# Optimization experiments

Hardware: AMD Instinct MI355X
Metric: run time of the kernel (lower is better)

## Reference

```python
import jax, jax.numpy as jnp
import numpy as np

MAX_NODES = 1024
FEAT = 64
HID = 32
B, S = 32, 4096


def setup_inputs() -> dict:
    key = jax.random.key(0)
    ks = jax.random.split(key, 9)
    flow_features = jax.random.normal(ks[0], (B, S, FEAT), dtype=jnp.float32)
    src_ips = jax.random.randint(ks[1], (B, S), 0, MAX_NODES, dtype=jnp.int32)
    dst_ips = jax.random.randint(ks[2], (B, S), 0, MAX_NODES, dtype=jnp.int32)
    flow_volumes = jax.random.uniform(ks[3], (B, S), dtype=jnp.float32)
    # learned parameters
    node_emb = jax.random.normal(ks[4], (MAX_NODES, FEAT), dtype=jnp.float32)
    W1 = jax.random.normal(ks[5], (2 * FEAT, HID), dtype=jnp.float32) * (1.0 / np.sqrt(2 * FEAT))
    b1 = jnp.zeros((HID,), dtype=jnp.float32)
    W2 = jax.random.normal(ks[6], (HID, 1), dtype=jnp.float32) * (1.0 / np.sqrt(HID))
    b2 = jnp.zeros((1,), dtype=jnp.float32)
    return {"flow_features": flow_features, "src_ips": src_ips, "dst_ips": dst_ips,
            "flow_volumes": flow_volumes, "node_emb": node_emb,
            "W1": W1, "b1": b1, "W2": W2, "b2": b2}


def reference(flow_features, src_ips, dst_ips, flow_volumes, node_emb, W1, b1, W2, b2):
    b_, s_, f_ = flow_features.shape
    n_ = node_emb.shape[0]
    bidx = jnp.arange(b_)[:, None]  # (B,1) broadcast over seq

    # ---- scatter-add flow features into destination nodes ----
    node_features = jnp.zeros((b_, n_, f_), dtype=flow_features.dtype)
    node_features = node_features.at[bidx, dst_ips].add(flow_features)
    # F.normalize(p=2, dim=-1): x / max(||x||, eps)
    norm = jnp.linalg.norm(node_features, axis=-1, keepdims=True)
    node_features = node_features / jnp.maximum(norm, 1e-12)

    # ---- gather embeddings, edge MLP, scatter weights into adjacency ----
    src_e = node_emb[src_ips]  # (B,S,F)
    dst_e = node_emb[dst_ips]  # (B,S,F)
    h = jax.nn.relu(jnp.concatenate([src_e, dst_e], axis=-1) @ W1 + b1)  # (B,S,32)
    edge_w = jax.nn.sigmoid((h @ W2 + b2)[..., 0])  # (B,S)
    vol_w = jax.nn.sigmoid(flow_volumes / 1000.0)
    w = edge_w * vol_w  # (B,S)

    adjacency = jnp.zeros((b_, n_, n_), dtype=flow_features.dtype)
    # semantics up to scatter ordering of colliding edges)
    adjacency = adjacency.at[bidx, src_ips, dst_ips].set(w)
    adjacency = adjacency.at[bidx, dst_ips, src_ips].set(w)
    return node_features, adjacency
```

## Files before the change

kernel.cpp:

```cpp
#include <hip/hip_runtime.h>
#include <cstdint>
#include <cstddef>

#define BB 32
#define SS 4096
#define FEAT_ 64
#define HID_ 32
#define NN 1024
#define RPB 8

#define EDGE_BLOCKS ((BB * SS) / 256)
#define NF_BLOCKS   ((BB * NN) / 32)

typedef int v4i __attribute__((ext_vector_type(4)));

__global__ void ab_kernel(const float* __restrict__ emb,
                          const float* __restrict__ W1,
                          const float* __restrict__ b1,
                          float* __restrict__ ab) {
    int idx = blockIdx.x * 256 + threadIdx.x;
    int n = idx >> 6;
    int c = idx & 63;
    int half = c >> 5, j = c & 31;
    const float* e = emb + (n << 6);
    const float* w = W1 + (half << 11) + j;
    float acc = half ? 0.0f : b1[j];
    #pragma unroll
    for (int k = 0; k < 64; ++k)
        acc = fmaf(e[k], w[k << 5], acc);
    ab[idx] = acc;
}

__global__ void nf_edge_kernel(const float* __restrict__ flow,
                               const int* __restrict__ src,
                               const int* __restrict__ dst,
                               const float* __restrict__ vol,
                               const float* __restrict__ ab,
                               const float* __restrict__ W2,
                               const float* __restrict__ b2,
                               float* __restrict__ nf,
                               float* __restrict__ wout) {
    if (blockIdx.x < EDGE_BLOCKS) {
        int i = blockIdx.x * 256 + threadIdx.x;
        int si = src[i], di = dst[i];
        const float4* As = (const float4*)(ab + (si << 6));
        const float4* Bd = (const float4*)(ab + (di << 6) + HID_);
        float dotv = b2[0];
        #pragma unroll
        for (int q = 0; q < 8; ++q) {
            float4 a  = As[q];
            float4 bv = Bd[q];
            float4 wv = *(const float4*)(W2 + (q << 2));
            dotv += fmaxf(a.x + bv.x, 0.0f) * wv.x;
            dotv += fmaxf(a.y + bv.y, 0.0f) * wv.y;
            dotv += fmaxf(a.z + bv.z, 0.0f) * wv.z;
            dotv += fmaxf(a.w + bv.w, 0.0f) * wv.w;
        }
        float edge_w = 1.0f / (1.0f + expf(-dotv));
        float vol_w  = 1.0f / (1.0f + expf(-vol[i] / 1000.0f));
        wout[i] = edge_w * vol_w;
        return;
    }

    int nb = blockIdx.x - EDGE_BLOCKS;
    int row0 = nb << 5;
    int b = row0 >> 10;
    __shared__ int sdst[SS];

    const int4* g = (const int4*)(dst + (size_t)b * SS);
    int4* sd4 = (int4*)sdst;
    for (int t = threadIdx.x; t < SS / 4; t += 256) sd4[t] = g[t];
    __syncthreads();

    int wave = threadIdx.x >> 6;
    int lane = threadIdx.x & 63;
    int r0 = row0 + (wave << 3);
    int node0 = r0 & (NN - 1);
    const float* fb = flow + ((size_t)b * SS << 6);

    float acc[8] = {0.f, 0.f, 0.f, 0.f, 0.f, 0.f, 0.f, 0.f};
    for (int s0 = 0; s0 < SS; s0 += 64) {
        int d = sdst[s0 + lane];
        #pragma unroll
        for (int j = 0; j < 8; ++j) {
            unsigned long long m = __ballot(d == node0 + j);
            while (m) {
                int bit = __ffsll((long long)m) - 1;
                m &= m - 1;
                acc[j] += fb[((s0 + bit) << 6) + lane];
            }
        }
    }

    #pragma unroll
    for (int j = 0; j < 8; ++j) {
        float ss = acc[j] * acc[j];
        #pragma unroll
        for (int off = 32; off > 0; off >>= 1) ss += __shfl_xor(ss, off, 64);
        float v = acc[j] / fmaxf(sqrtf(ss), 1e-12f);
        __builtin_nontemporal_store(v, &nf[((size_t)(r0 + j) << 6) + lane]);
    }
}

__global__ void adj_dense_kernel(const int* __restrict__ src,
                                 const int* __restrict__ dst,
                                 const float* __restrict__ wbuf,
                                 float* __restrict__ adj) {
    int b  = blockIdx.x >> 7;
    int r0 = (blockIdx.x & 127) << 3;
    int tid = threadIdx.x;

    __shared__ int D[RPB * NN];

    const int* sb = src + (size_t)b * SS;
    const int* db = dst + (size_t)b * SS;
    int svr[16], dvr[16];
    #pragma unroll
    for (int i = 0; i < 16; ++i) {
        svr[i] = sb[tid + (i << 8)];
        dvr[i] = db[tid + (i << 8)];
    }

    int4* D4 = (int4*)D;
    int4 z; z.x = z.y = z.z = z.w = 0;
    #pragma unroll
    for (int i = 0; i < RPB * NN / 4 / 256; ++i) D4[tid + i * 256] = z;
    __syncthreads();

    #pragma unroll
    for (int i = 0; i < 16; ++i) {
        int s = tid + (i << 8);
        unsigned lr1 = (unsigned)(svr[i] - r0);
        if (lr1 < RPB) atomicMax(&D[(lr1 << 10) + dvr[i]], s + 1);
        unsigned lr2 = (unsigned)(dvr[i] - r0);
        if (lr2 < RPB) atomicMax(&D[(lr2 << 10) + svr[i]], SS + s + 1);
    }
    __syncthreads();

    const float* wb = wbuf + (size_t)b * SS;
    #pragma unroll
    for (int i = 0; i < 16; ++i) {
        int s = tid + (i << 8);
        unsigned lr1 = (unsigned)(svr[i] - r0);
        unsigned lr2 = (unsigned)(dvr[i] - r0);
        if ((lr1 < RPB) | (lr2 < RPB)) {
            int wbits = __float_as_int(wb[s]);
            if (lr1 < RPB && D[(lr1 << 10) + dvr[i]] == s + 1)
                D[(lr1 << 10) + dvr[i]] = wbits;
            if (lr2 < RPB && D[(lr2 << 10) + svr[i]] == SS + s + 1)
                D[(lr2 << 10) + svr[i]] = wbits;
        }
    }
    __syncthreads();

    const v4i* Df = (const v4i*)D;
    v4i* out = (v4i*)(adj + ((size_t)b * NN + r0) * NN);
    #pragma unroll
    for (int i = 0; i < RPB * NN / 4 / 256; ++i)
        __builtin_nontemporal_store(Df[tid + i * 256], &out[tid + i * 256]);
}

extern "C" void kernel_launch(void* const* d_in, const int* in_sizes, int n_in,
                              void* d_out, int out_size, void* d_ws, size_t ws_size,
                              hipStream_t stream) {
    const float* flow = (const float*)d_in[0];
    const int*   src  = (const int*)d_in[1];
    const int*   dst  = (const int*)d_in[2];
    const float* vol  = (const float*)d_in[3];
    const float* emb  = (const float*)d_in[4];
    const float* W1   = (const float*)d_in[5];
    const float* b1   = (const float*)d_in[6];
    const float* W2   = (const float*)d_in[7];
    const float* b2   = (const float*)d_in[8];

    float* nf   = (float*)d_out;
    float* adj  = nf + (size_t)BB * NN * FEAT_;
    float* wbuf = (float*)d_ws;

    float* ab;
    if (ws_size >= (size_t)(BB * SS + NN * 64) * sizeof(float))
        ab = wbuf + (size_t)BB * SS;
    else
        ab = adj + (size_t)BB * NN * NN - (size_t)NN * 64;

    ab_kernel<<<(NN * 64) / 256, 256, 0, stream>>>(emb, W1, b1, ab);
    nf_edge_kernel<<<EDGE_BLOCKS + NF_BLOCKS, 256, 0, stream>>>(
        flow, src, dst, vol, ab, W2, b2, nf, wbuf);
    adj_dense_kernel<<<BB * (NN / RPB), 256, 0, stream>>>(src, dst, wbuf, adj);
}
```

Measured before the change: 225.5 us.

## Build CSR edge lists per node and fuse scatter-add with adjacency construction

A setup kernel computes the embedding projections and builds per-batch CSR (counting sort) edge lists keyed by dst and by src. The dst list is insertion-sorted so sums keep sequence order. A single fused kernel then computes node features by walking only the incident edges, and fills adjacency tiles by visiting only the edges in each row range, computing edge weights on demand. This replaces the O(S) ballot scan per row group and the full-edge scan per adjacency block, and drops the separate edge-weight pass and a kernel launch. In exchange it adds sorting overhead, serial insertion sort in some threads, and a larger workspace requirement, with the old path kept as a fallback.

```diff
diff --git a/kernel.cpp b/kernel.cpp
--- a/kernel.cpp
+++ b/kernel.cpp
@@ -14,20 +14,238 @@
 
 typedef int v4i __attribute__((ext_vector_type(4)));
 
+__device__ __forceinline__ float edge_weight(const float* __restrict__ ab,
+                                             const float* __restrict__ W2,
+                                             float b2v, int src_n, int dst_n,
+                                             float volv) {
+    const float4* As = (const float4*)(ab + (src_n << 6));
+    const float4* Bd = (const float4*)(ab + (dst_n << 6) + HID_);
+    float dotv = b2v;
+    #pragma unroll
+    for (int q = 0; q < 8; ++q) {
+        float4 a  = As[q];
+        float4 bv = Bd[q];
+        float4 wv = *(const float4*)(W2 + (q << 2));
+        dotv += fmaxf(a.x + bv.x, 0.0f) * wv.x;
+        dotv += fmaxf(a.y + bv.y, 0.0f) * wv.y;
+        dotv += fmaxf(a.z + bv.z, 0.0f) * wv.z;
+        dotv += fmaxf(a.w + bv.w, 0.0f) * wv.w;
+    }
+    float edge_w = 1.0f / (1.0f + expf(-dotv));
+    float vol_w  = 1.0f / (1.0f + expf(-volv / 1000.0f));
+    return edge_w * vol_w;
+}
+
+__global__ void setup_kernel(const float* __restrict__ emb,
+                             const float* __restrict__ W1,
+                             const float* __restrict__ b1,
+                             const int* __restrict__ src,
+                             const int* __restrict__ dst,
+                             float* __restrict__ ab,
+                             int* __restrict__ offD, int* __restrict__ idxD,
+                             int* __restrict__ offS, int* __restrict__ idxS) {
+    int t = threadIdx.x;
+    if (blockIdx.x < 256) {
+        int idx = blockIdx.x * 256 + t;
+        int n = idx >> 6, c = idx & 63;
+        int half = c >> 5, j = c & 31;
+        const float* e = emb + (n << 6);
+        const float* w = W1 + (half << 11) + j;
+        float acc = half ? 0.0f : b1[j];
+        #pragma unroll
+        for (int k = 0; k < 64; ++k) acc = fmaf(e[k], w[k << 5], acc);
+        ab[idx] = acc;
+        return;
+    }
+
+    int blk = blockIdx.x - 256;
+    int dir = blk >> 5;
+    int b   = blk & 31;
+    const int* keyg = (dir ? src : dst) + (size_t)b * SS;
+    const int* othg = (dir ? dst : src) + (size_t)b * SS;
+    int* offg = (dir ? offS : offD) + b * (NN + 1);
+    int* idxg = (dir ? idxS : idxD) + b * SS;
+
+    int kv[16], ov[16];
+    #pragma unroll
+    for (int i = 0; i < 16; ++i) {
+        kv[i] = keyg[t + (i << 8)];
+        ov[i] = othg[t + (i << 8)];
+    }
+
+    __shared__ int cnt[NN];
+    __shared__ int wtot[4];
+    #pragma unroll
+    for (int i = 0; i < 4; ++i) cnt[(t << 2) + i] = 0;
+    __syncthreads();
+    #pragma unroll
+    for (int i = 0; i < 16; ++i) atomicAdd(&cnt[kv[i]], 1);
+    __syncthreads();
+
+    int c0 = cnt[t * 4], c1 = cnt[t * 4 + 1], c2 = cnt[t * 4 + 2], c3 = cnt[t * 4 + 3];
+    int p1 = c0 + c1, p2 = p1 + c2, p3 = p2 + c3;
+    int x = p3;
+    int lane = t & 63, wv = t >> 6;
+    #pragma unroll
+    for (int d = 1; d < 64; d <<= 1) {
+        int y = __shfl_up(x, d, 64);
+        if (lane >= d) x += y;
+    }
+    if (lane == 63) wtot[wv] = x;
+    __syncthreads();
+    int wbase = 0;
+    #pragma unroll
+    for (int w2 = 0; w2 < 4; ++w2) if (w2 < wv) wbase += wtot[w2];
+    int e0 = wbase + x - p3;
+    int e1 = e0 + c0, e2 = e0 + p1, e3 = e0 + p2;
+    offg[t * 4 + 0] = e0; offg[t * 4 + 1] = e1;
+    offg[t * 4 + 2] = e2; offg[t * 4 + 3] = e3;
+    if (t == 255) offg[NN] = SS;
+    __syncthreads();
+    cnt[t * 4] = e0; cnt[t * 4 + 1] = e1; cnt[t * 4 + 2] = e2; cnt[t * 4 + 3] = e3;
+    __syncthreads();
+
+    #pragma unroll
+    for (int i = 0; i < 16; ++i) {
+        int s = t + (i << 8);
+        int pos = atomicAdd(&cnt[kv[i]], 1);
+        idxg[pos] = (int)((unsigned)s | ((unsigned)ov[i] << 12) | ((unsigned)kv[i] << 22));
+    }
+
+    if (dir == 0) {
+        __syncthreads();
+        int beg[4] = {e0, e1, e2, e3};
+        int len[4] = {c0, c1, c2, c3};
+        #pragma unroll
+        for (int q = 0; q < 4; ++q) {
+            int lo = beg[q], hi = beg[q] + len[q];
+            for (int p = lo + 1; p < hi; ++p) {
+                int v = idxg[p];
+                int sq = v & 4095;
+                int r = p - 1;
+                while (r >= lo && (idxg[r] & 4095) > sq) { idxg[r + 1] = idxg[r]; --r; }
+                idxg[r + 1] = v;
+            }
+        }
+    }
+}
+
+__global__ void fused_kernel(const float* __restrict__ flow,
+                             const float* __restrict__ vol,
+                             const float* __restrict__ ab,
+                             const float* __restrict__ W2,
+                             const float* __restrict__ b2,
+                             const int* __restrict__ offD, const int* __restrict__ idxD,
+                             const int* __restrict__ offS, const int* __restrict__ idxS,
+                             float* __restrict__ nf,
+                             float* __restrict__ adj) {
+    int g = blockIdx.x / 5;
+    int r = blockIdx.x - g * 5;
+    int t = threadIdx.x;
+    __shared__ int D[RPB * NN];
+
+    if (r == 4) {
+        int nb = g;
+        int b = nb >> 5;
+        int row0 = (nb & 31) << 5;
+        int wave = t >> 6, lane = t & 63;
+        int r0 = row0 + (wave << 3);
+        const float* fb = flow + ((size_t)b * SS << 6);
+        const int* offb = offD + b * (NN + 1);
+        const int* idxb = idxD + b * SS;
+        #pragma unroll
+        for (int j = 0; j < 8; ++j) {
+            int row = r0 + j;
+            int eb = offb[row], ee = offb[row + 1];
+            float a = 0.f;
+            int e = eb;
+            for (; e + 4 <= ee; e += 4) {
+                int s0 = idxb[e]     & 4095, s1 = idxb[e + 1] & 4095;
+                int s2 = idxb[e + 2] & 4095, s3 = idxb[e + 3] & 4095;
+                float v0 = fb[(s0 << 6) + lane], v1 = fb[(s1 << 6) + lane];
+                float v2 = fb[(s2 << 6) + lane], v3 = fb[(s3 << 6) + lane];
+                a = (((a + v0) + v1) + v2) + v3;
+            }
+            for (; e < ee; ++e) {
+                int s = idxb[e] & 4095;
+                a += fb[(s << 6) + lane];
+            }
+            float ssum = a * a;
+            #pragma unroll
+            for (int off = 32; off > 0; off >>= 1) ssum += __shfl_xor(ssum, off, 64);
+            float v = a / fmaxf(sqrtf(ssum), 1e-12f);
+            __builtin_nontemporal_store(
+                v, &nf[((size_t)(b * NN + row) << 6) + lane]);
+        }
+        return;
+    }
+
+    int aidx = g * 4 + r;
+    int b  = aidx >> 7;
+    int r0 = (aidx & 127) << 3;
+
+    const int* offSb = offS + b * (NN + 1);
+    const int* offDb = offD + b * (NN + 1);
+    const int* idxSb = idxS + b * SS;
+    const int* idxDb = idxD + b * SS;
+    int begS = offSb[r0], cntS = offSb[r0 + RPB] - begS;
+    int begD = offDb[r0], cntD = offDb[r0 + RPB] - begD;
+
+    int4* D4 = (int4*)D;
+    int4 z; z.x = z.y = z.z = z.w = 0;
+    #pragma unroll
+    for (int i = 0; i < RPB * NN / 4 / 256; ++i) D4[t + i * 256] = z;
+    __syncthreads();
+
+    for (int i = t; i < cntS; i += 256) {
+        unsigned v = (unsigned)idxSb[begS + i];
+        int s = (int)(v & 4095u); int col = (int)((v >> 12) & 1023u); int row = (int)(v >> 22);
+        atomicMax(&D[((row - r0) << 10) + col], s + 1);
+    }
+    for (int i = t; i < cntD; i += 256) {
+        unsigned v = (unsigned)idxDb[begD + i];
+        int s = (int)(v & 4095u); int col = (int)((v >> 12) & 1023u); int row = (int)(v >> 22);
+        atomicMax(&D[((row - r0) << 10) + col], SS + s + 1);
+    }
+    __syncthreads();
+
+    const float* volb = vol + (size_t)b * SS;
+    float b2v = b2[0];
+    for (int i = t; i < cntS; i += 256) {
+        unsigned v = (unsigned)idxSb[begS + i];
+        int s = (int)(v & 4095u); int col = (int)((v >> 12) & 1023u); int row = (int)(v >> 22);
+        int cell = ((row - r0) << 10) + col;
+        if (D[cell] == s + 1)
+            D[cell] = __float_as_int(edge_weight(ab, W2, b2v, row, col, volb[s]));
+    }
+    for (int i = t; i < cntD; i += 256) {
+        unsigned v = (unsigned)idxDb[begD + i];
+        int s = (int)(v & 4095u); int col = (int)((v >> 12) & 1023u); int row = (int)(v >> 22);
+        int cell = ((row - r0) << 10) + col;
+        if (D[cell] == SS + s + 1)
+            D[cell] = __float_as_int(edge_weight(ab, W2, b2v, col, row, volb[s]));
+    }
+    __syncthreads();
+
+    const v4i* Df = (const v4i*)D;
+    v4i* out = (v4i*)(adj + ((size_t)b * NN + r0) * NN);
+    #pragma unroll
+    for (int i = 0; i < RPB * NN / 4 / 256; ++i)
+        __builtin_nontemporal_store(Df[t + i * 256], &out[t + i * 256]);
+}
+
 __global__ void ab_kernel(const float* __restrict__ emb,
                           const float* __restrict__ W1,
                           const float* __restrict__ b1,
                           float* __restrict__ ab) {
     int idx = blockIdx.x * 256 + threadIdx.x;
-    int n = idx >> 6;
-    int c = idx & 63;
+    int n = idx >> 6, c = idx & 63;
     int half = c >> 5, j = c & 31;
     const float* e = emb + (n << 6);
     const float* w = W1 + (half << 11) + j;
     float acc = half ? 0.0f : b1[j];
     #pragma unroll
-    for (int k = 0; k < 64; ++k)
-        acc = fmaf(e[k], w[k << 5], acc);
+    for (int k = 0; k < 64; ++k) acc = fmaf(e[k], w[k << 5], acc);
     ab[idx] = acc;
 }
 
@@ -43,42 +261,23 @@
     if (blockIdx.x < EDGE_BLOCKS) {
         int i = blockIdx.x * 256 + threadIdx.x;
         int si = src[i], di = dst[i];
-        const float4* As = (const float4*)(ab + (si << 6));
-        const float4* Bd = (const float4*)(ab + (di << 6) + HID_);
-        float dotv = b2[0];
-        #pragma unroll
-        for (int q = 0; q < 8; ++q) {
-            float4 a  = As[q];
-            float4 bv = Bd[q];
-            float4 wv = *(const float4*)(W2 + (q << 2));
-            dotv += fmaxf(a.x + bv.x, 0.0f) * wv.x;
-            dotv += fmaxf(a.y + bv.y, 0.0f) * wv.y;
-            dotv += fmaxf(a.z + bv.z, 0.0f) * wv.z;
-            dotv += fmaxf(a.w + bv.w, 0.0f) * wv.w;
-        }
-        float edge_w = 1.0f / (1.0f + expf(-dotv));
-        float vol_w  = 1.0f / (1.0f + expf(-vol[i] / 1000.0f));
-        wout[i] = edge_w * vol_w;
+        float w = edge_weight(ab, W2, b2[0], si, di, vol[i]);
+        wout[i] = w;
         return;
     }
-
     int nb = blockIdx.x - EDGE_BLOCKS;
     int row0 = nb << 5;
     int b = row0 >> 10;
     __shared__ int sdst[SS];
-
     const int4* g = (const int4*)(dst + (size_t)b * SS);
     int4* sd4 = (int4*)sdst;
     for (int t = threadIdx.x; t < SS / 4; t += 256) sd4[t] = g[t];
     __syncthreads();
-
-    int wave = threadIdx.x >> 6;
-    int lane = threadIdx.x & 63;
+    int wave = threadIdx.x >> 6, lane = threadIdx.x & 63;
     int r0 = row0 + (wave << 3);
     int node0 = r0 & (NN - 1);
     const float* fb = flow + ((size_t)b * SS << 6);
-
-    float acc[8] = {0.f, 0.f, 0.f, 0.f, 0.f, 0.f, 0.f, 0.f};
+    float acc[8] = {0.f,0.f,0.f,0.f,0.f,0.f,0.f,0.f};
     for (int s0 = 0; s0 < SS; s0 += 64) {
         int d = sdst[s0 + lane];
         #pragma unroll
@@ -91,7 +290,6 @@
             }
         }
     }
-
     #pragma unroll
     for (int j = 0; j < 8; ++j) {
         float ss = acc[j] * acc[j];
@@ -109,24 +307,17 @@
     int b  = blockIdx.x >> 7;
     int r0 = (blockIdx.x & 127) << 3;
     int tid = threadIdx.x;
-
     __shared__ int D[RPB * NN];
-
     const int* sb = src + (size_t)b * SS;
     const int* db = dst + (size_t)b * SS;
     int svr[16], dvr[16];
     #pragma unroll
-    for (int i = 0; i < 16; ++i) {
-        svr[i] = sb[tid + (i << 8)];
-        dvr[i] = db[tid + (i << 8)];
-    }
-
+    for (int i = 0; i < 16; ++i) { svr[i] = sb[tid + (i << 8)]; dvr[i] = db[tid + (i << 8)]; }
     int4* D4 = (int4*)D;
     int4 z; z.x = z.y = z.z = z.w = 0;
     #pragma unroll
     for (int i = 0; i < RPB * NN / 4 / 256; ++i) D4[tid + i * 256] = z;
     __syncthreads();
-
     #pragma unroll
     for (int i = 0; i < 16; ++i) {
         int s = tid + (i << 8);
@@ -136,7 +327,6 @@
         if (lr2 < RPB) atomicMax(&D[(lr2 << 10) + svr[i]], SS + s + 1);
     }
     __syncthreads();
-
     const float* wb = wbuf + (size_t)b * SS;
     #pragma unroll
     for (int i = 0; i < 16; ++i) {
@@ -145,14 +335,11 @@
         unsigned lr2 = (unsigned)(dvr[i] - r0);
         if ((lr1 < RPB) | (lr2 < RPB)) {
             int wbits = __float_as_int(wb[s]);
-            if (lr1 < RPB && D[(lr1 << 10) + dvr[i]] == s + 1)
-                D[(lr1 << 10) + dvr[i]] = wbits;
-            if (lr2 < RPB && D[(lr2 << 10) + svr[i]] == SS + s + 1)
-                D[(lr2 << 10) + svr[i]] = wbits;
+            if (lr1 < RPB && D[(lr1 << 10) + dvr[i]] == s + 1) D[(lr1 << 10) + dvr[i]] = wbits;
+            if (lr2 < RPB && D[(lr2 << 10) + svr[i]] == SS + s + 1) D[(lr2 << 10) + svr[i]] = wbits;
         }
     }
     __syncthreads();
-
     const v4i* Df = (const v4i*)D;
     v4i* out = (v4i*)(adj + ((size_t)b * NN + r0) * NN);
     #pragma unroll
@@ -173,16 +360,30 @@
     const float* W2   = (const float*)d_in[7];
     const float* b2   = (const float*)d_in[8];
 
-    float* nf   = (float*)d_out;
-    float* adj  = nf + (size_t)BB * NN * FEAT_;
+    float* nf  = (float*)d_out;
+    float* adj = nf + (size_t)BB * NN * FEAT_;
+
+    size_t need = ((size_t)NN * 64 + 2 * (size_t)BB * (NN + 1) + 2 * (size_t)BB * SS)
+                  * sizeof(float);
+    if (ws_size >= need) {
+        float* ab  = (float*)d_ws;
+        int* offD = (int*)(ab + NN * 64);
+        int* idxD = offD + BB * (NN + 1);
+        int* offS = idxD + BB * SS;
+        int* idxS = offS + BB * (NN + 1);
+        setup_kernel<<<320, 256, 0, stream>>>(emb, W1, b1, src, dst,
+                                              ab, offD, idxD, offS, idxS);
+        fused_kernel<<<5120, 256, 0, stream>>>(flow, vol, ab, W2, b2,
+                                               offD, idxD, offS, idxS, nf, adj);
+        return;
+    }
+
     float* wbuf = (float*)d_ws;
-
     float* ab;
     if (ws_size >= (size_t)(BB * SS + NN * 64) * sizeof(float))
         ab = wbuf + (size_t)BB * SS;
     else
         ab = adj + (size_t)BB * NN * NN - (size_t)NN * 64;
-
     ab_kernel<<<(NN * 64) / 256, 256, 0, stream>>>(emb, W1, b1, ab);
     nf_edge_kernel<<<EDGE_BLOCKS + NF_BLOCKS, 256, 0, stream>>>(
         flow, src, dst, vol, ab, W2, b2, nf, wbuf);
```

Result: slower. 252.5 us (+12.0%).

## Fuse node-feature and adjacency kernels, compute edge weights inside adjacency blocks

Applied to the files above, without the earlier changes.

Merges the node-feature scatter and dense adjacency construction into a single launch, interleaving one node-feature block per four adjacency blocks. Edge weights are no longer precomputed into a workspace buffer; each adjacency block evaluates the edge MLP on demand for edges touching its rows. This removes one launch, the weight buffer round trip, and serialization between the two phases. In exchange, edges are evaluated about twice (once per endpoint row block), and the node-feature blocks now share the larger shared-memory footprint, which could lower occupancy.

```diff
diff --git a/kernel.cpp b/kernel.cpp
--- a/kernel.cpp
+++ b/kernel.cpp
@@ -14,21 +14,149 @@
 
 typedef int v4i __attribute__((ext_vector_type(4)));
 
+__device__ __forceinline__ float edge_weight(const float* __restrict__ ab,
+                                             const float* __restrict__ W2,
+                                             float b2v, int src_n, int dst_n,
+                                             float volv) {
+    const float4* As = (const float4*)(ab + (src_n << 6));
+    const float4* Bd = (const float4*)(ab + (dst_n << 6) + HID_);
+    float dotv = b2v;
+    #pragma unroll
+    for (int q = 0; q < 8; ++q) {
+        float4 a  = As[q];
+        float4 bv = Bd[q];
+        float4 wv = *(const float4*)(W2 + (q << 2));
+        dotv += fmaxf(a.x + bv.x, 0.0f) * wv.x;
+        dotv += fmaxf(a.y + bv.y, 0.0f) * wv.y;
+        dotv += fmaxf(a.z + bv.z, 0.0f) * wv.z;
+        dotv += fmaxf(a.w + bv.w, 0.0f) * wv.w;
+    }
+    float edge_w = 1.0f / (1.0f + expf(-dotv));
+    float vol_w  = 1.0f / (1.0f + expf(-volv / 1000.0f));
+    return edge_w * vol_w;
+}
+
 __global__ void ab_kernel(const float* __restrict__ emb,
                           const float* __restrict__ W1,
                           const float* __restrict__ b1,
                           float* __restrict__ ab) {
     int idx = blockIdx.x * 256 + threadIdx.x;
-    int n = idx >> 6;
-    int c = idx & 63;
+    int n = idx >> 6, c = idx & 63;
     int half = c >> 5, j = c & 31;
     const float* e = emb + (n << 6);
     const float* w = W1 + (half << 11) + j;
     float acc = half ? 0.0f : b1[j];
     #pragma unroll
-    for (int k = 0; k < 64; ++k)
-        acc = fmaf(e[k], w[k << 5], acc);
+    for (int k = 0; k < 64; ++k) acc = fmaf(e[k], w[k << 5], acc);
     ab[idx] = acc;
+}
+
+__global__ void fused2_kernel(const float* __restrict__ flow,
+                              const int* __restrict__ src,
+                              const int* __restrict__ dst,
+                              const float* __restrict__ vol,
+                              const float* __restrict__ ab,
+                              const float* __restrict__ W2,
+                              const float* __restrict__ b2,
+                              float* __restrict__ nf,
+                              float* __restrict__ adj) {
+    int g = blockIdx.x / 5;
+    int r = blockIdx.x - g * 5;
+    int t = threadIdx.x;
+    __shared__ int D[RPB * NN];
+
+    if (r == 4) {
+        int nb = g;
+        int row0 = nb << 5;
+        int b = row0 >> 10;
+        int* sdst = D;
+
+        const int4* gsrc = (const int4*)(dst + (size_t)b * SS);
+        int4* sd4 = (int4*)sdst;
+        for (int i = t; i < SS / 4; i += 256) sd4[i] = gsrc[i];
+        __syncthreads();
+
+        int wave = t >> 6, lane = t & 63;
+        int r0 = row0 + (wave << 3);
+        int node0 = r0 & (NN - 1);
+        const float* fb = flow + ((size_t)b * SS << 6);
+
+        float acc[8] = {0.f,0.f,0.f,0.f,0.f,0.f,0.f,0.f};
+        for (int s0 = 0; s0 < SS; s0 += 64) {
+            int d = sdst[s0 + lane];
+            #pragma unroll
+            for (int j = 0; j < 8; ++j) {
+                unsigned long long m = __ballot(d == node0 + j);
+                while (m) {
+                    int bit = __ffsll((long long)m) - 1;
+                    m &= m - 1;
+                    acc[j] += fb[((s0 + bit) << 6) + lane];
+                }
+            }
+        }
+        #pragma unroll
+        for (int j = 0; j < 8; ++j) {
+            float ss = acc[j] * acc[j];
+            #pragma unroll
+            for (int off = 32; off > 0; off >>= 1) ss += __shfl_xor(ss, off, 64);
+            float v = acc[j] / fmaxf(sqrtf(ss), 1e-12f);
+            __builtin_nontemporal_store(v, &nf[((size_t)(r0 + j) << 6) + lane]);
+        }
+        return;
+    }
+
+    int aidx = g * 4 + r;
+    int b  = aidx >> 7;
+    int r0 = (aidx & 127) << 3;
+
+    const int* sb = src + (size_t)b * SS;
+    const int* db = dst + (size_t)b * SS;
+    int svr[16], dvr[16];
+    #pragma unroll
+    for (int i = 0; i < 16; ++i) {
+        svr[i] = sb[t + (i << 8)];
+        dvr[i] = db[t + (i << 8)];
+    }
+
+    int4* D4 = (int4*)D;
+    int4 z; z.x = z.y = z.z = z.w = 0;
+    #pragma unroll
+    for (int i = 0; i < RPB * NN / 4 / 256; ++i) D4[t + i * 256] = z;
+    __syncthreads();
+
+    #pragma unroll
+    for (int i = 0; i < 16; ++i) {
+        int s = t + (i << 8);
+        unsigned lr1 = (unsigned)(svr[i] - r0);
+        if (lr1 < RPB) atomicMax(&D[(lr1 << 10) + dvr[i]], s + 1);
+        unsigned lr2 = (unsigned)(dvr[i] - r0);
+        if (lr2 < RPB) atomicMax(&D[(lr2 << 10) + svr[i]], SS + s + 1);
+    }
+    __syncthreads();
+
+    const float* volb = vol + (size_t)b * SS;
+    float b2v = b2[0];
+    #pragma unroll
+    for (int i = 0; i < 16; ++i) {
+        int s = t + (i << 8);
+        unsigned lr1 = (unsigned)(svr[i] - r0);
+        unsigned lr2 = (unsigned)(dvr[i] - r0);
+        if ((lr1 < RPB) | (lr2 < RPB)) {
+            float w = edge_weight(ab, W2, b2v, svr[i], dvr[i], volb[s]);
+            int wbits = __float_as_int(w);
+            if (lr1 < RPB && D[(lr1 << 10) + dvr[i]] == s + 1)
+                D[(lr1 << 10) + dvr[i]] = wbits;
+            if (lr2 < RPB && D[(lr2 << 10) + svr[i]] == SS + s + 1)
+                D[(lr2 << 10) + svr[i]] = wbits;
+        }
+    }
+    __syncthreads();
+
+    const v4i* Df = (const v4i*)D;
+    v4i* out = (v4i*)(adj + ((size_t)b * NN + r0) * NN);
+    #pragma unroll
+    for (int i = 0; i < RPB * NN / 4 / 256; ++i)
+        __builtin_nontemporal_store(Df[t + i * 256], &out[t + i * 256]);
 }
 
 __global__ void nf_edge_kernel(const float* __restrict__ flow,
@@ -42,43 +170,23 @@
                                float* __restrict__ wout) {
     if (blockIdx.x < EDGE_BLOCKS) {
         int i = blockIdx.x * 256 + threadIdx.x;
-        int si = src[i], di = dst[i];
-        const float4* As = (const float4*)(ab + (si << 6));
-        const float4* Bd = (const float4*)(ab + (di << 6) + HID_);
-        float dotv = b2[0];
-        #pragma unroll
-        for (int q = 0; q < 8; ++q) {
-            float4 a  = As[q];
-            float4 bv = Bd[q];
-            float4 wv = *(const float4*)(W2 + (q << 2));
-            dotv += fmaxf(a.x + bv.x, 0.0f) * wv.x;
-            dotv += fmaxf(a.y + bv.y, 0.0f) * wv.y;
-            dotv += fmaxf(a.z + bv.z, 0.0f) * wv.z;
-            dotv += fmaxf(a.w + bv.w, 0.0f) * wv.w;
-        }
-        float edge_w = 1.0f / (1.0f + expf(-dotv));
-        float vol_w  = 1.0f / (1.0f + expf(-vol[i] / 1000.0f));
-        wout[i] = edge_w * vol_w;
+        float w = edge_weight(ab, W2, b2[0], src[i], dst[i], vol[i]);
+        wout[i] = w;
         return;
     }
-
     int nb = blockIdx.x - EDGE_BLOCKS;
     int row0 = nb << 5;
     int b = row0 >> 10;
     __shared__ int sdst[SS];
-
     const int4* g = (const int4*)(dst + (size_t)b * SS);
     int4* sd4 = (int4*)sdst;
     for (int t = threadIdx.x; t < SS / 4; t += 256) sd4[t] = g[t];
     __syncthreads();
-
-    int wave = threadIdx.x >> 6;
-    int lane = threadIdx.x & 63;
+    int wave = threadIdx.x >> 6, lane = threadIdx.x & 63;
     int r0 = row0 + (wave << 3);
     int node0 = r0 & (NN - 1);
     const float* fb = flow + ((size_t)b * SS << 6);
-
-    float acc[8] = {0.f, 0.f, 0.f, 0.f, 0.f, 0.f, 0.f, 0.f};
+    float acc[8] = {0.f,0.f,0.f,0.f,0.f,0.f,0.f,0.f};
     for (int s0 = 0; s0 < SS; s0 += 64) {
         int d = sdst[s0 + lane];
         #pragma unroll
@@ -91,7 +199,6 @@
             }
         }
     }
-
     #pragma unroll
     for (int j = 0; j < 8; ++j) {
         float ss = acc[j] * acc[j];
@@ -109,24 +216,17 @@
     int b  = blockIdx.x >> 7;
     int r0 = (blockIdx.x & 127) << 3;
     int tid = threadIdx.x;
-
     __shared__ int D[RPB * NN];
-
     const int* sb = src + (size_t)b * SS;
     const int* db = dst + (size_t)b * SS;
     int svr[16], dvr[16];
     #pragma unroll
-    for (int i = 0; i < 16; ++i) {
-        svr[i] = sb[tid + (i << 8)];
-        dvr[i] = db[tid + (i << 8)];
-    }
-
+    for (int i = 0; i < 16; ++i) { svr[i] = sb[tid + (i << 8)]; dvr[i] = db[tid + (i << 8)]; }
     int4* D4 = (int4*)D;
     int4 z; z.x = z.y = z.z = z.w = 0;
     #pragma unroll
     for (int i = 0; i < RPB * NN / 4 / 256; ++i) D4[tid + i * 256] = z;
     __syncthreads();
-
     #pragma unroll
     for (int i = 0; i < 16; ++i) {
         int s = tid + (i << 8);
@@ -136,7 +236,6 @@
         if (lr2 < RPB) atomicMax(&D[(lr2 << 10) + svr[i]], SS + s + 1);
     }
     __syncthreads();
-
     const float* wb = wbuf + (size_t)b * SS;
     #pragma unroll
     for (int i = 0; i < 16; ++i) {
@@ -145,14 +244,11 @@
         unsigned lr2 = (unsigned)(dvr[i] - r0);
         if ((lr1 < RPB) | (lr2 < RPB)) {
             int wbits = __float_as_int(wb[s]);
-            if (lr1 < RPB && D[(lr1 << 10) + dvr[i]] == s + 1)
-                D[(lr1 << 10) + dvr[i]] = wbits;
-            if (lr2 < RPB && D[(lr2 << 10) + svr[i]] == SS + s + 1)
-                D[(lr2 << 10) + svr[i]] = wbits;
-        }
-    }
-    __syncthreads();
-
+            if (lr1 < RPB && D[(lr1 << 10) + dvr[i]] == s + 1) D[(lr1 << 10) + dvr[i]] = wbits;
+            if (lr2 < RPB && D[(lr2 << 10) + svr[i]] == SS + s + 1) D[(lr2 << 10) + svr[i]] = wbits;
+        }
+    }
+    __syncthreads();
     const v4i* Df = (const v4i*)D;
     v4i* out = (v4i*)(adj + ((size_t)b * NN + r0) * NN);
     #pragma unroll
@@ -173,16 +269,23 @@
     const float* W2   = (const float*)d_in[7];
     const float* b2   = (const float*)d_in[8];
 
-    float* nf   = (float*)d_out;
-    float* adj  = nf + (size_t)BB * NN * FEAT_;
+    float* nf  = (float*)d_out;
+    float* adj = nf + (size_t)BB * NN * FEAT_;
+
+    if (ws_size >= (size_t)NN * 64 * sizeof(float)) {
+        float* ab = (float*)d_ws;
+        ab_kernel<<<(NN * 64) / 256, 256, 0, stream>>>(emb, W1, b1, ab);
+        fused2_kernel<<<5 * BB * (NN / RPB) / 4, 256, 0, stream>>>(
+            flow, src, dst, vol, ab, W2, b2, nf, adj);
+        return;
+    }
+
     float* wbuf = (float*)d_ws;
-
     float* ab;
     if (ws_size >= (size_t)(BB * SS + NN * 64) * sizeof(float))
         ab = wbuf + (size_t)BB * SS;
     else
         ab = adj + (size_t)BB * NN * NN - (size_t)NN * 64;
-
     ab_kernel<<<(NN * 64) / 256, 256, 0, stream>>>(emb, W1, b1, ab);
     nf_edge_kernel<<<EDGE_BLOCKS + NF_BLOCKS, 256, 0, stream>>>(
         flow, src, dst, vol, ab, W2, b2, nf, wbuf);
```

New measurement: 299.5 us. 32.8% more time.
